# Optimization experiments

Measured on AMD Instinct MI355X. Metric: run time of the kernel, lower is better.

## Reference

```python
import jax, jax.numpy as jnp
import numpy as np

B, IN, OUT, NUM_F = 131072, 128, 128, 8


def setup_inputs() -> dict:
    key = jax.random.key(0)
    ks = jax.random.split(key, 6)
    x = jax.random.normal(ks[0], (B, IN), dtype=jnp.float32)
    grid = jnp.arange(NUM_F, dtype=jnp.float32) + 1.0            # nn.Parameter(arange(num_f)+1)
    base_weight = jax.random.normal(ks[1], (OUT, IN), dtype=jnp.float32) * 0.05
    scale_sp = jnp.ones((OUT,), dtype=jnp.float32)
    coef = jax.random.uniform(ks[2], (IN, NUM_F), dtype=jnp.float32)  # torch.rand
    # Conv1d(in=IN*NUM_F, out=OUT*NUM_F, k=1, groups=NUM_F) == per-frequency [OUT, IN] matmul
    fan_in = IN  # per-group in-channels * kernel_size(1)
    bound = 1.0 / np.sqrt(fan_in)
    conv_w = jax.random.uniform(ks[3], (NUM_F, OUT, IN), dtype=jnp.float32,
                                minval=-bound, maxval=bound)
    conv_b = jax.random.uniform(ks[4], (NUM_F, OUT), dtype=jnp.float32,
                                minval=-bound, maxval=bound)
    return {"x": x, "grid": grid, "base_weight": base_weight,
            "scale_sp": scale_sp, "coef": coef, "conv_w": conv_w, "conv_b": conv_b}


def reference(x, grid, base_weight, scale_sp, coef, conv_w, conv_b):
    # base path: SiLU(x) @ W_base^T  -> [B, OUT]
    base_out = jax.nn.silu(x) @ base_weight.T
    # Fourier basis: sin(grid_f * x_i) -> [B, F, I]
    s = jnp.sin(x[:, None, :] * grid[None, :, None])
    # coef [I, F] broadcast-multiplied per (i, f)
    s = s * coef.T[None, :, :]                      # [B, F, I]
    # grouped 1x1 conv == per-frequency matmul, plus per-(f, o) bias
    spline = jnp.einsum('bfi,foi->bfo', s, conv_w) + conv_b[None, :, :]  # [B, F, OUT]
    spline_out = spline.sum(axis=1) * scale_sp      # [B, OUT]
    return base_out + spline_out
```

## Files before the change

### kernel.cpp

```cpp
#include <hip/hip_runtime.h>
#include <stdint.h>

#define NCHUNK 9
#define IN_DIM 128
#define OUT_DIM 128
#define NUM_F 8
#define B_TOTAL 131072

#define WBASE_ELEMS (OUT_DIM * IN_DIM)
#define WSIN_ELEMS (8 * OUT_DIM * IN_DIM)
#define SLICE 16384

typedef _Float16 hf16x8 __attribute__((ext_vector_type(8)));
typedef float floatx16 __attribute__((ext_vector_type(16)));

typedef __attribute__((address_space(1))) const unsigned int gas_u32;
typedef __attribute__((address_space(3))) unsigned int las_u32;

__device__ __forceinline__ unsigned short f2h_rn(float f) {
  _Float16 h = (_Float16)f;
  return __builtin_bit_cast(unsigned short, h);
}

__global__ void skan_prep(const float* __restrict__ base_w,
                          const float* __restrict__ scale_sp,
                          const float* __restrict__ coef,
                          const float* __restrict__ conv_w,
                          const float* __restrict__ conv_b,
                          unsigned short* __restrict__ Wbase,
                          unsigned short* __restrict__ Wsin,
                          float* __restrict__ bias) {
  int b = blockIdx.x;
  int i = threadIdx.x;
  int j = i & 7, q2 = (i >> 3) & 1;
  if (b < NCHUNK * OUT_DIM) {
    int c = b >> 7;
    int o = b & 127;
    if (c == 0) {
      float v = base_w[o * IN_DIM + i];
      Wbase[((i >> 4) * 2 + q2) * 1024 + o * 8 + j] = f2h_rn(v);
    } else {
      int f = c - 1;
      float v = conv_w[(f * OUT_DIM + o) * IN_DIM + i] * coef[i * NUM_F + f] * scale_sp[o];
      Wsin[((i >> 4) * 16 + f * 2 + q2) * 1024 + o * 8 + j] = f2h_rn(v);
    }
  } else {
    float s = 0.f;
#pragma unroll
    for (int f = 0; f < NUM_F; ++f) s += conv_b[f * OUT_DIM + i];
    bias[i] = s * scale_sp[i];
  }
}

__device__ __forceinline__ hf16x8 hpack(const float* v) {
  union { unsigned u[4]; hf16x8 f; } r;
  r.u[0] = __builtin_bit_cast(unsigned, __builtin_amdgcn_cvt_pkrtz(v[0], v[1]));
  r.u[1] = __builtin_bit_cast(unsigned, __builtin_amdgcn_cvt_pkrtz(v[2], v[3]));
  r.u[2] = __builtin_bit_cast(unsigned, __builtin_amdgcn_cvt_pkrtz(v[4], v[5]));
  r.u[3] = __builtin_bit_cast(unsigned, __builtin_amdgcn_cvt_pkrtz(v[6], v[7]));
  return r.f;
}

__device__ __forceinline__ float silu(float v) {
  return v * __builtin_amdgcn_rcpf(1.f + __expf(-v));
}

__global__ __launch_bounds__(256, 3)
void skan_main(const float* __restrict__ x,
               const unsigned short* __restrict__ Wbase,
               const unsigned short* __restrict__ Wsin,
               const float* __restrict__ bias,
               float* __restrict__ out) {
  __shared__ unsigned short sB[SLICE];

  const int tid  = threadIdx.x;
  const int lane = tid & 63;
  const int w    = tid >> 6;
  const int wr   = w >> 1;
  const int wc   = w & 1;
  const int m    = lane & 31;
  const int q2   = lane >> 5;
  const int rowBase = blockIdx.x * 128 + wr * 64;

  const int colOff = wc * 512 + m * 8;

  floatx16 acc[2][2];
#pragma unroll
  for (int mt = 0; mt < 2; ++mt)
#pragma unroll
    for (int nt = 0; nt < 2; ++nt)
#pragma unroll
      for (int e = 0; e < 16; ++e) acc[mt][nt][e] = 0.f;

  const float* xr0 = x + (size_t)(rowBase + m) * IN_DIM;
  const float* xr1 = xr0 + 32 * IN_DIM;

#pragma unroll 1
  for (int p = 0; p < 8; ++p) {
    {
      const char* src = (const char*)(Wsin + p * SLICE);
      char* dst = (char*)sB;
      int off = tid * 16;
#pragma unroll
      for (int it = 0; it < 8; ++it) {
        __builtin_amdgcn_global_load_lds((gas_u32*)(src + off), (las_u32*)(dst + off),
                                         16, 0, 0);
        off += 4096;
      }
    }

    float xv[2][8];
#pragma unroll
    for (int mt = 0; mt < 2; ++mt) {
      const float* xr = mt ? xr1 : xr0;
      float4 a = *(const float4*)(xr + p * 16 + q2 * 8);
      float4 b = *(const float4*)(xr + p * 16 + q2 * 8 + 4);
      xv[mt][0] = a.x; xv[mt][1] = a.y; xv[mt][2] = a.z; xv[mt][3] = a.w;
      xv[mt][4] = b.x; xv[mt][5] = b.y; xv[mt][6] = b.z; xv[mt][7] = b.w;
    }

    {
      int4 Bb[2];
#pragma unroll
      for (int nt = 0; nt < 2; ++nt)
        Bb[nt] = *(const int4*)(Wbase + (p * 2 + q2) * 1024 + colOff + nt * 256);
      float sv[16];
#pragma unroll
      for (int mt = 0; mt < 2; ++mt)
#pragma unroll
        for (int j = 0; j < 8; ++j) sv[mt * 8 + j] = silu(xv[mt][j]);
      hf16x8 a0 = hpack(&sv[0]);
      hf16x8 a1 = hpack(&sv[8]);
#pragma unroll
      for (int nt = 0; nt < 2; ++nt) {
        hf16x8 bf = __builtin_bit_cast(hf16x8, Bb[nt]);
        acc[0][nt] = __builtin_amdgcn_mfma_f32_32x32x16_f16(a0, bf, acc[0][nt], 0, 0, 0);
        acc[1][nt] = __builtin_amdgcn_mfma_f32_32x32x16_f16(a1, bf, acc[1][nt], 0, 0, 0);
      }
    }

    __syncthreads();

    {
      float sp[16], spp[16], c2[16];
#pragma unroll
      for (int mt = 0; mt < 2; ++mt)
#pragma unroll
        for (int j = 0; j < 8; ++j) {
          int v = mt * 8 + j;
          float xx = xv[mt][j];
          sp[v]  = __sinf(xx);
          c2[v]  = 2.f * __cosf(xx);
          spp[v] = 0.f;
        }

#pragma unroll
      for (int c = 1; c <= 8; ++c) {
        hf16x8 Bf[2];
        const unsigned short* bp = sB + ((c - 1) * 2 + q2) * 1024 + colOff;
#pragma unroll
        for (int nt = 0; nt < 2; ++nt)
          Bf[nt] = *(const hf16x8*)(bp + nt * 256);

        if (c >= 2) {
#pragma unroll
          for (int v = 0; v < 16; ++v) {
            float t = __builtin_fmaf(c2[v], sp[v], -spp[v]);
            spp[v] = sp[v];
            sp[v] = t;
          }
        }
        hf16x8 a0 = hpack(&sp[0]);
        hf16x8 a1 = hpack(&sp[8]);
#pragma unroll
        for (int nt = 0; nt < 2; ++nt) {
          acc[0][nt] = __builtin_amdgcn_mfma_f32_32x32x16_f16(a0, Bf[nt], acc[0][nt], 0, 0, 0);
          acc[1][nt] = __builtin_amdgcn_mfma_f32_32x32x16_f16(a1, Bf[nt], acc[1][nt], 0, 0, 0);
        }
      }
    }

    __syncthreads();
  }

#pragma unroll
  for (int mt = 0; mt < 2; ++mt) {
    float* obase = out + (size_t)(rowBase + mt * 32) * OUT_DIM + wc * 64 + m;
#pragma unroll
    for (int nt = 0; nt < 2; ++nt) {
      float bv = bias[wc * 64 + nt * 32 + m];
#pragma unroll
      for (int e = 0; e < 16; ++e) {
        int rl = (e & 3) + 8 * (e >> 2) + 4 * q2;
        obase[(size_t)rl * OUT_DIM + nt * 32] = acc[mt][nt][e] + bv;
      }
    }
  }
}

extern "C" void kernel_launch(void* const* d_in, const int* in_sizes, int n_in,
                              void* d_out, int out_size, void* d_ws, size_t ws_size,
                              hipStream_t stream) {
  const float* x      = (const float*)d_in[0];
  const float* base_w = (const float*)d_in[2];
  const float* scale  = (const float*)d_in[3];
  const float* coef   = (const float*)d_in[4];
  const float* conv_w = (const float*)d_in[5];
  const float* conv_b = (const float*)d_in[6];

  unsigned short* Wbase = (unsigned short*)d_ws;
  unsigned short* Wsin  = Wbase + WBASE_ELEMS;
  float* bias = (float*)(Wsin + WSIN_ELEMS);
  float* out  = (float*)d_out;

  skan_prep<<<NCHUNK * OUT_DIM + 1, 128, 0, stream>>>(base_w, scale, coef,
                                                      conv_w, conv_b, Wbase, Wsin, bias);
  skan_main<<<B_TOTAL / 128, 256, 0, stream>>>(x, Wbase, Wsin, bias, out);
}
```

Baseline: 160.7 us.

## Retile waves to 32 rows by all 128 columns to stop duplicate basis math

Each wave now owns 32 full rows and all 128 output columns (four 32x32 MFMA tiles), instead of a 64x64 quarter of the block tile. In the old layout, two waves loaded the same x rows and each recomputed SiLU, sin/cos and the Chebyshev recurrence for them. The new layout does that elementwise work and the x loads once per row. In exchange, each wave reads twice as many B fragments from LDS and global Wbase per step, so shared-memory bandwidth pressure goes up.

```diff
diff --git a/kernel.cpp b/kernel.cpp
--- a/kernel.cpp
+++ b/kernel.cpp
@@ -76,24 +76,19 @@
   const int tid  = threadIdx.x;
   const int lane = tid & 63;
   const int w    = tid >> 6;
-  const int wr   = w >> 1;
-  const int wc   = w & 1;
   const int m    = lane & 31;
   const int q2   = lane >> 5;
-  const int rowBase = blockIdx.x * 128 + wr * 64;
+  const int waveRow = blockIdx.x * 128 + w * 32;
 
-  const int colOff = wc * 512 + m * 8;
+  const int colOff = m * 8;
 
-  floatx16 acc[2][2];
+  floatx16 acc[4];
 #pragma unroll
-  for (int mt = 0; mt < 2; ++mt)
+  for (int nt = 0; nt < 4; ++nt)
 #pragma unroll
-    for (int nt = 0; nt < 2; ++nt)
-#pragma unroll
-      for (int e = 0; e < 16; ++e) acc[mt][nt][e] = 0.f;
+    for (int e = 0; e < 16; ++e) acc[nt][e] = 0.f;
 
-  const float* xr0 = x + (size_t)(rowBase + m) * IN_DIM;
-  const float* xr1 = xr0 + 32 * IN_DIM;
+  const float* xr = x + (size_t)(waveRow + m) * IN_DIM;
 
 #pragma unroll 1
   for (int p = 0; p < 8; ++p) {
@@ -109,91 +104,76 @@
       }
     }
 
-    float xv[2][8];
-#pragma unroll
-    for (int mt = 0; mt < 2; ++mt) {
-      const float* xr = mt ? xr1 : xr0;
+    float xv[8];
+    {
       float4 a = *(const float4*)(xr + p * 16 + q2 * 8);
       float4 b = *(const float4*)(xr + p * 16 + q2 * 8 + 4);
-      xv[mt][0] = a.x; xv[mt][1] = a.y; xv[mt][2] = a.z; xv[mt][3] = a.w;
-      xv[mt][4] = b.x; xv[mt][5] = b.y; xv[mt][6] = b.z; xv[mt][7] = b.w;
+      xv[0] = a.x; xv[1] = a.y; xv[2] = a.z; xv[3] = a.w;
+      xv[4] = b.x; xv[5] = b.y; xv[6] = b.z; xv[7] = b.w;
     }
 
     {
-      int4 Bb[2];
+      int4 Bb[4];
 #pragma unroll
-      for (int nt = 0; nt < 2; ++nt)
+      for (int nt = 0; nt < 4; ++nt)
         Bb[nt] = *(const int4*)(Wbase + (p * 2 + q2) * 1024 + colOff + nt * 256);
-      float sv[16];
+      float sv[8];
 #pragma unroll
-      for (int mt = 0; mt < 2; ++mt)
+      for (int j = 0; j < 8; ++j) sv[j] = silu(xv[j]);
+      hf16x8 a0 = hpack(sv);
 #pragma unroll
-        for (int j = 0; j < 8; ++j) sv[mt * 8 + j] = silu(xv[mt][j]);
-      hf16x8 a0 = hpack(&sv[0]);
-      hf16x8 a1 = hpack(&sv[8]);
-#pragma unroll
-      for (int nt = 0; nt < 2; ++nt) {
+      for (int nt = 0; nt < 4; ++nt) {
         hf16x8 bf = __builtin_bit_cast(hf16x8, Bb[nt]);
-        acc[0][nt] = __builtin_amdgcn_mfma_f32_32x32x16_f16(a0, bf, acc[0][nt], 0, 0, 0);
-        acc[1][nt] = __builtin_amdgcn_mfma_f32_32x32x16_f16(a1, bf, acc[1][nt], 0, 0, 0);
+        acc[nt] = __builtin_amdgcn_mfma_f32_32x32x16_f16(a0, bf, acc[nt], 0, 0, 0);
       }
     }
 
     __syncthreads();
 
     {
-      float sp[16], spp[16], c2[16];
+      float sp[8], spp[8], c2[8];
 #pragma unroll
-      for (int mt = 0; mt < 2; ++mt)
-#pragma unroll
-        for (int j = 0; j < 8; ++j) {
-          int v = mt * 8 + j;
-          float xx = xv[mt][j];
-          sp[v]  = __sinf(xx);
-          c2[v]  = 2.f * __cosf(xx);
-          spp[v] = 0.f;
-        }
+      for (int j = 0; j < 8; ++j) {
+        float xx = xv[j];
+        sp[j]  = __sinf(xx);
+        c2[j]  = 2.f * __cosf(xx);
+        spp[j] = 0.f;
+      }
 
 #pragma unroll
       for (int c = 1; c <= 8; ++c) {
-        hf16x8 Bf[2];
+        hf16x8 Bf[4];
         const unsigned short* bp = sB + ((c - 1) * 2 + q2) * 1024 + colOff;
 #pragma unroll
-        for (int nt = 0; nt < 2; ++nt)
+        for (int nt = 0; nt < 4; ++nt)
           Bf[nt] = *(const hf16x8*)(bp + nt * 256);
 
         if (c >= 2) {
 #pragma unroll
-          for (int v = 0; v < 16; ++v) {
-            float t = __builtin_fmaf(c2[v], sp[v], -spp[v]);
-            spp[v] = sp[v];
-            sp[v] = t;
+          for (int j = 0; j < 8; ++j) {
+            float t = __builtin_fmaf(c2[j], sp[j], -spp[j]);
+            spp[j] = sp[j];
+            sp[j] = t;
           }
         }
-        hf16x8 a0 = hpack(&sp[0]);
-        hf16x8 a1 = hpack(&sp[8]);
+        hf16x8 a0 = hpack(sp);
 #pragma unroll
-        for (int nt = 0; nt < 2; ++nt) {
-          acc[0][nt] = __builtin_amdgcn_mfma_f32_32x32x16_f16(a0, Bf[nt], acc[0][nt], 0, 0, 0);
-          acc[1][nt] = __builtin_amdgcn_mfma_f32_32x32x16_f16(a1, Bf[nt], acc[1][nt], 0, 0, 0);
-        }
+        for (int nt = 0; nt < 4; ++nt)
+          acc[nt] = __builtin_amdgcn_mfma_f32_32x32x16_f16(a0, Bf[nt], acc[nt], 0, 0, 0);
       }
     }
 
     __syncthreads();
   }
 
+  float* obase = out + (size_t)waveRow * OUT_DIM + m;
 #pragma unroll
-  for (int mt = 0; mt < 2; ++mt) {
-    float* obase = out + (size_t)(rowBase + mt * 32) * OUT_DIM + wc * 64 + m;
+  for (int nt = 0; nt < 4; ++nt) {
+    float bv = bias[nt * 32 + m];
 #pragma unroll
-    for (int nt = 0; nt < 2; ++nt) {
-      float bv = bias[wc * 64 + nt * 32 + m];
-#pragma unroll
-      for (int e = 0; e < 16; ++e) {
-        int rl = (e & 3) + 8 * (e >> 2) + 4 * q2;
-        obase[(size_t)rl * OUT_DIM + nt * 32] = acc[mt][nt][e] + bv;
-      }
+    for (int e = 0; e < 16; ++e) {
+      int rl = (e & 3) + 8 * (e >> 2) + 4 * q2;
+      obase[(size_t)rl * OUT_DIM + nt * 32] = acc[nt][e] + bv;
     }
   }
 }
```

Result: no change. 158.9 us (-1.1%).

## Enlarge row tile to 512 and stage half of sine weights per sync

Applied to the files above, without the earlier changes.

The block grows from 256 to 512 threads, and each block now covers 512 rows with every wave computing all 128 output columns. The full sine-weight set is staged into LDS in two 128 KB halves, so there are only a couple of barriers per block instead of two per frequency slice. Each weight byte loaded from global memory is reused across four times as many rows. The cost is 128 KB of dynamic LDS, which limits occupancy to one block per CU, and roughly double the accumulator registers per wave.

```diff
diff --git a/kernel.cpp b/kernel.cpp
--- a/kernel.cpp
+++ b/kernel.cpp
@@ -9,7 +9,7 @@
 
 #define WBASE_ELEMS (OUT_DIM * IN_DIM)
 #define WSIN_ELEMS (8 * OUT_DIM * IN_DIM)
-#define SLICE 16384
+#define HALF_ELEMS 65536
 
 typedef _Float16 hf16x8 __attribute__((ext_vector_type(8)));
 typedef float floatx16 __attribute__((ext_vector_type(16)));
@@ -65,30 +65,28 @@
   return v * __builtin_amdgcn_rcpf(1.f + __expf(-v));
 }
 
-__global__ __launch_bounds__(256, 3)
+__global__ __launch_bounds__(512, 2)
 void skan_main(const float* __restrict__ x,
                const unsigned short* __restrict__ Wbase,
                const unsigned short* __restrict__ Wsin,
                const float* __restrict__ bias,
                float* __restrict__ out) {
-  __shared__ unsigned short sB[SLICE];
+  extern __shared__ unsigned short sB[];
 
   const int tid  = threadIdx.x;
   const int lane = tid & 63;
   const int w    = tid >> 6;
-  const int wr   = w >> 1;
-  const int wc   = w & 1;
   const int m    = lane & 31;
   const int q2   = lane >> 5;
-  const int rowBase = blockIdx.x * 128 + wr * 64;
-
-  const int colOff = wc * 512 + m * 8;
-
-  floatx16 acc[2][2];
+  const int rowBase = blockIdx.x * 512 + w * 64;
+
+  const int colOff = m * 8;
+
+  floatx16 acc[2][4];
 #pragma unroll
   for (int mt = 0; mt < 2; ++mt)
 #pragma unroll
-    for (int nt = 0; nt < 2; ++nt)
+    for (int nt = 0; nt < 4; ++nt)
 #pragma unroll
       for (int e = 0; e < 16; ++e) acc[mt][nt][e] = 0.f;
 
@@ -96,52 +94,40 @@
   const float* xr1 = xr0 + 32 * IN_DIM;
 
 #pragma unroll 1
-  for (int p = 0; p < 8; ++p) {
+  for (int kh = 0; kh < 2; ++kh) {
+    if (kh) __syncthreads();
+
     {
-      const char* src = (const char*)(Wsin + p * SLICE);
+      const char* src = (const char*)(Wsin + kh * HALF_ELEMS);
       char* dst = (char*)sB;
       int off = tid * 16;
 #pragma unroll
-      for (int it = 0; it < 8; ++it) {
+      for (int it = 0; it < 16; ++it) {
         __builtin_amdgcn_global_load_lds((gas_u32*)(src + off), (las_u32*)(dst + off),
                                          16, 0, 0);
-        off += 4096;
-      }
-    }
-
-    float xv[2][8];
-#pragma unroll
-    for (int mt = 0; mt < 2; ++mt) {
-      const float* xr = mt ? xr1 : xr0;
-      float4 a = *(const float4*)(xr + p * 16 + q2 * 8);
-      float4 b = *(const float4*)(xr + p * 16 + q2 * 8 + 4);
-      xv[mt][0] = a.x; xv[mt][1] = a.y; xv[mt][2] = a.z; xv[mt][3] = a.w;
-      xv[mt][4] = b.x; xv[mt][5] = b.y; xv[mt][6] = b.z; xv[mt][7] = b.w;
-    }
-
-    {
-      int4 Bb[2];
-#pragma unroll
-      for (int nt = 0; nt < 2; ++nt)
+        off += 8192;
+      }
+    }
+
+#pragma unroll
+    for (int ph = 0; ph < 4; ++ph) {
+      const int p = kh * 4 + ph;
+
+      float xv[2][8];
+#pragma unroll
+      for (int mt = 0; mt < 2; ++mt) {
+        const float* xr = mt ? xr1 : xr0;
+        float4 a = *(const float4*)(xr + p * 16 + q2 * 8);
+        float4 b = *(const float4*)(xr + p * 16 + q2 * 8 + 4);
+        xv[mt][0] = a.x; xv[mt][1] = a.y; xv[mt][2] = a.z; xv[mt][3] = a.w;
+        xv[mt][4] = b.x; xv[mt][5] = b.y; xv[mt][6] = b.z; xv[mt][7] = b.w;
+      }
+
+      int4 Bb[4];
+#pragma unroll
+      for (int nt = 0; nt < 4; ++nt)
         Bb[nt] = *(const int4*)(Wbase + (p * 2 + q2) * 1024 + colOff + nt * 256);
-      float sv[16];
-#pragma unroll
-      for (int mt = 0; mt < 2; ++mt)
-#pragma unroll
-        for (int j = 0; j < 8; ++j) sv[mt * 8 + j] = silu(xv[mt][j]);
-      hf16x8 a0 = hpack(&sv[0]);
-      hf16x8 a1 = hpack(&sv[8]);
-#pragma unroll
-      for (int nt = 0; nt < 2; ++nt) {
-        hf16x8 bf = __builtin_bit_cast(hf16x8, Bb[nt]);
-        acc[0][nt] = __builtin_amdgcn_mfma_f32_32x32x16_f16(a0, bf, acc[0][nt], 0, 0, 0);
-        acc[1][nt] = __builtin_amdgcn_mfma_f32_32x32x16_f16(a1, bf, acc[1][nt], 0, 0, 0);
-      }
-    }
-
-    __syncthreads();
-
-    {
+
       float sp[16], spp[16], c2[16];
 #pragma unroll
       for (int mt = 0; mt < 2; ++mt)
@@ -154,12 +140,14 @@
           spp[v] = 0.f;
         }
 
+      if (ph == 0) __syncthreads();
+
 #pragma unroll
       for (int c = 1; c <= 8; ++c) {
-        hf16x8 Bf[2];
-        const unsigned short* bp = sB + ((c - 1) * 2 + q2) * 1024 + colOff;
-#pragma unroll
-        for (int nt = 0; nt < 2; ++nt)
+        hf16x8 Bf[4];
+        const unsigned short* bp = sB + (ph * 16 + (c - 1) * 2 + q2) * 1024 + colOff;
+#pragma unroll
+        for (int nt = 0; nt < 4; ++nt)
           Bf[nt] = *(const hf16x8*)(bp + nt * 256);
 
         if (c >= 2) {
@@ -173,22 +161,36 @@
         hf16x8 a0 = hpack(&sp[0]);
         hf16x8 a1 = hpack(&sp[8]);
 #pragma unroll
-        for (int nt = 0; nt < 2; ++nt) {
+        for (int nt = 0; nt < 4; ++nt) {
           acc[0][nt] = __builtin_amdgcn_mfma_f32_32x32x16_f16(a0, Bf[nt], acc[0][nt], 0, 0, 0);
           acc[1][nt] = __builtin_amdgcn_mfma_f32_32x32x16_f16(a1, Bf[nt], acc[1][nt], 0, 0, 0);
         }
       }
-    }
-
-    __syncthreads();
+
+      {
+        float sv[16];
+#pragma unroll
+        for (int mt = 0; mt < 2; ++mt)
+#pragma unroll
+          for (int j = 0; j < 8; ++j) sv[mt * 8 + j] = silu(xv[mt][j]);
+        hf16x8 a0 = hpack(&sv[0]);
+        hf16x8 a1 = hpack(&sv[8]);
+#pragma unroll
+        for (int nt = 0; nt < 4; ++nt) {
+          hf16x8 bf = __builtin_bit_cast(hf16x8, Bb[nt]);
+          acc[0][nt] = __builtin_amdgcn_mfma_f32_32x32x16_f16(a0, bf, acc[0][nt], 0, 0, 0);
+          acc[1][nt] = __builtin_amdgcn_mfma_f32_32x32x16_f16(a1, bf, acc[1][nt], 0, 0, 0);
+        }
+      }
+    }
   }
 
 #pragma unroll
   for (int mt = 0; mt < 2; ++mt) {
-    float* obase = out + (size_t)(rowBase + mt * 32) * OUT_DIM + wc * 64 + m;
-#pragma unroll
-    for (int nt = 0; nt < 2; ++nt) {
-      float bv = bias[wc * 64 + nt * 32 + m];
+    float* obase = out + (size_t)(rowBase + mt * 32) * OUT_DIM + m;
+#pragma unroll
+    for (int nt = 0; nt < 4; ++nt) {
+      float bv = bias[nt * 32 + m];
 #pragma unroll
       for (int e = 0; e < 16; ++e) {
         int rl = (e & 3) + 8 * (e >> 2) + 4 * q2;
@@ -213,7 +215,15 @@
   float* bias = (float*)(Wsin + WSIN_ELEMS);
   float* out  = (float*)d_out;
 
+  static bool attr_done = false;
+  if (!attr_done) {
+    hipFuncSetAttribute((const void*)skan_main,
+                        hipFuncAttributeMaxDynamicSharedMemorySize,
+                        HALF_ELEMS * 2);
+    attr_done = true;
+  }
+
   skan_prep<<<NCHUNK * OUT_DIM + 1, 128, 0, stream>>>(base_w, scale, coef,
                                                       conv_w, conv_b, Wbase, Wsin, bias);
-  skan_main<<<B_TOTAL / 128, 256, 0, stream>>>(x, Wbase, Wsin, bias, out);
-}
+  skan_main<<<B_TOTAL / 512, 512, HALF_ELEMS * 2, stream>>>(x, Wbase, Wsin, bias, out);
+}
```

Measured after the change: 150.9 us. 6.1% less time.
